# Optimization experiments

Measured on AMD Instinct MI355X. Metric: run time of the kernel, lower is better.

## Reference

```python
import jax, jax.numpy as jnp
import numpy as np

N, T, D, H = 4, 2048, 1024, 16
DK = D // H

def setup_inputs() -> dict:
    key = jax.random.key(0)
    k1, k2, k3 = jax.random.split(key, 3)
    z = jax.random.normal(k1, (N, T, D), dtype=jnp.float32)
    Wqkv = jax.random.normal(k2, (D, 3 * D), dtype=jnp.float32) * 0.01
    Wout = jax.random.normal(k3, (D, D), dtype=jnp.float32) * 0.01
    return {"z": z, "Wqkv": Wqkv, "Wout": Wout}

def reference(z, Wqkv, Wout):
    n, t, d = z.shape
    scale = DK ** -0.5
    qkv = z @ Wqkv  # [N,T,3D]
    q, k, v = jnp.split(qkv, 3, axis=-1)
    # [N,T,D] -> [N,H,T,dk]
    q = q.reshape(n, t, H, DK).transpose(0, 2, 1, 3)
    k = k.reshape(n, t, H, DK).transpose(0, 2, 1, 3)
    v = v.reshape(n, t, H, DK).transpose(0, 2, 1, 3)
    attn = jnp.einsum('nhqd,nhkd->nhqk', q, k) * scale
    causal = jnp.tril(jnp.ones((t, t), dtype=bool))
    attn = jnp.where(causal, attn, -jnp.inf)
    attn = jax.nn.softmax(attn, axis=-1)
    out = jnp.einsum('nhqk,nhkd->nhqd', attn, v)  # [N,H,T,dk]
    out = out.transpose(0, 2, 1, 3).reshape(n, t, d)
    return out @ Wout
```

## Files before the change

### kernel.cpp

```cpp
#include <hip/hip_runtime.h>
#include <hip/hip_bf16.h>

typedef __bf16 bf16;
typedef __bf16 bf16x8 __attribute__((ext_vector_type(8)));
typedef float f32x4 __attribute__((ext_vector_type(4)));

#define N_B 4
#define T_S 2048
#define D_M 1024
#define H_N 16
#define D_K 64
#define D3 3072
#define NEG_BIG (-1e30f)
#define QSCALE 0.18033688011112042f

#if __has_builtin(__builtin_amdgcn_exp2f)
#define EXP2(x) __builtin_amdgcn_exp2f(x)
#else
#define EXP2(x) exp2f(x)
#endif

__device__ __forceinline__ void gload_lds16(const bf16* g, bf16* l) {
    __builtin_amdgcn_global_load_lds((const __attribute__((address_space(1))) void*)g,
                                     (__attribute__((address_space(3))) void*)l, 16, 0, 0);
}

__device__ __forceinline__ bool probe_fp32(const void* p) {
    const unsigned int* w = (const unsigned int*)p;
    int weird = 0;
#pragma unroll
    for (int i = 0; i < 16; ++i) {
        unsigned int v = w[i];
        unsigned int e = (v >> 7) & 0xFFu;
        if ((v & 0xFFFFu) != 0u && (e < 100u || e > 140u)) weird++;
    }
    return weird >= 4;
}

__global__ __launch_bounds__(256) void prep(const void* __restrict__ z, bf16* __restrict__ zb,
                                            const void* __restrict__ Wqkv, bf16* __restrict__ WqkvT,
                                            const void* __restrict__ Wout, bf16* __restrict__ WoutT) {
    __shared__ bf16 tile[32][33];
    const int b = blockIdx.x;
    const int t = threadIdx.x;

    if (b < 4096) {
        const int i = (b * 256 + t) * 8;
        if (probe_fp32(z)) {
            const float* zf = (const float*)z;
            float4 u0 = *(const float4*)(zf + i);
            float4 u1 = *(const float4*)(zf + i + 4);
            union { uint4 q; bf16 h[8]; } pk;
            pk.h[0] = (bf16)u0.x; pk.h[1] = (bf16)u0.y;
            pk.h[2] = (bf16)u0.z; pk.h[3] = (bf16)u0.w;
            pk.h[4] = (bf16)u1.x; pk.h[5] = (bf16)u1.y;
            pk.h[6] = (bf16)u1.z; pk.h[7] = (bf16)u1.w;
            *(uint4*)(zb + i) = pk.q;
        } else {
            *(uint4*)(zb + i) = ((const uint4*)z)[b * 256 + t];
        }
        return;
    }

    const void* in; bf16* out; int R, C, c0, r0;
    if (b < 7168) {
        int idx = b - 4096;
        in = Wqkv; out = WqkvT; R = 1024; C = 3072;
        c0 = (idx % 96) * 32; r0 = (idx / 96) * 32;
    } else {
        int idx = b - 7168;
        in = Wout; out = WoutT; R = 1024; C = 1024;
        c0 = (idx & 31) * 32; r0 = (idx >> 5) * 32;
    }
    const int tx = t & 31, ty = t >> 5;
    if (probe_fp32(in)) {
        const float* inf_ = (const float*)in;
        for (int i = 0; i < 4; ++i)
            tile[ty + i * 8][tx] = (bf16)inf_[(size_t)(r0 + ty + i * 8) * C + c0 + tx];
    } else {
        const bf16* inb = (const bf16*)in;
        for (int i = 0; i < 4; ++i)
            tile[ty + i * 8][tx] = inb[(size_t)(r0 + ty + i * 8) * C + c0 + tx];
    }
    __syncthreads();
    for (int i = 0; i < 4; ++i)
        out[(size_t)(c0 + ty + i * 8) * R + r0 + tx] = tile[tx][ty + i * 8];
}

__global__ __launch_bounds__(512, 2) void gemmq(const bf16* __restrict__ A,
                                                const bf16* __restrict__ Bt,
                                                void* __restrict__ C,
                                                bf16* __restrict__ Kf,
                                                bf16* __restrict__ Vf,
                                                int M, int N, int K,
                                                int modeC, int nbx) {
    __shared__ bf16 As[2][256 * 64];
    __shared__ bf16 Bs[2][256 * 64];

    const int nwg = gridDim.x;
    const int per = nwg >> 3;
    const int b0 = blockIdx.x;
    const int bid = (b0 & 7) * per + (b0 >> 3);
    const int by = bid / nbx;
    const int bx = bid - by * nbx;
    const int m0 = by * 256, n0 = bx * 256;

    const int t = threadIdx.x;
    const int w = t >> 6, lane = t & 63, quad = lane >> 4, l15 = lane & 15;
    const int wr = (w >> 2) * 128;
    const int wc = (w & 3) * 64;
    const int sr = t >> 3;
    const int sg = ((t & 7) ^ (sr & 7)) * 8;
    const int xorL = (l15 & 7) * 8;
    const int ldsOff = w * 512;

    const bf16* ag0 = A + (size_t)(m0 + sr) * K + sg;
    const bf16* ag1 = A + (size_t)(m0 + 64 + sr) * K + sg;
    const bf16* ag2 = A + (size_t)(m0 + 128 + sr) * K + sg;
    const bf16* ag3 = A + (size_t)(m0 + 192 + sr) * K + sg;
    const bf16* bg0 = Bt + (size_t)(n0 + sr) * K + sg;
    const bf16* bg1 = Bt + (size_t)(n0 + 64 + sr) * K + sg;
    const bf16* bg2 = Bt + (size_t)(n0 + 128 + sr) * K + sg;
    const bf16* bg3 = Bt + (size_t)(n0 + 192 + sr) * K + sg;

    f32x4 acc[8][4];
    const f32x4 zero4 = {0.f, 0.f, 0.f, 0.f};
#pragma unroll
    for (int i = 0; i < 8; ++i)
#pragma unroll
        for (int j = 0; j < 4; ++j) acc[i][j] = zero4;

    const int nt = K >> 6;

    gload_lds16(ag0, &As[0][0 * 4096 + ldsOff]);
    gload_lds16(ag1, &As[0][1 * 4096 + ldsOff]);
    gload_lds16(ag2, &As[0][2 * 4096 + ldsOff]);
    gload_lds16(ag3, &As[0][3 * 4096 + ldsOff]);
    gload_lds16(bg0, &Bs[0][0 * 4096 + ldsOff]);
    gload_lds16(bg1, &Bs[0][1 * 4096 + ldsOff]);
    gload_lds16(bg2, &Bs[0][2 * 4096 + ldsOff]);
    gload_lds16(bg3, &Bs[0][3 * 4096 + ldsOff]);

    for (int tt = 0; tt < nt; ++tt) {
        const int s = tt & 1;
        __builtin_amdgcn_sched_barrier(0);
        if (tt + 1 < nt) {
            const int kn = (tt + 1) << 6;
            bf16* Ad = As[s ^ 1];
            bf16* Bd = Bs[s ^ 1];
            gload_lds16(ag0 + kn, Ad + 0 * 4096 + ldsOff);
            gload_lds16(ag1 + kn, Ad + 1 * 4096 + ldsOff);
            gload_lds16(ag2 + kn, Ad + 2 * 4096 + ldsOff);
            gload_lds16(ag3 + kn, Ad + 3 * 4096 + ldsOff);
            gload_lds16(bg0 + kn, Bd + 0 * 4096 + ldsOff);
            gload_lds16(bg1 + kn, Bd + 1 * 4096 + ldsOff);
            gload_lds16(bg2 + kn, Bd + 2 * 4096 + ldsOff);
            gload_lds16(bg3 + kn, Bd + 3 * 4096 + ldsOff);
            asm volatile("s_waitcnt vmcnt(8)" ::: "memory");
        } else {
            asm volatile("s_waitcnt vmcnt(0)" ::: "memory");
        }
        __builtin_amdgcn_sched_barrier(0);
        __builtin_amdgcn_s_barrier();
        __builtin_amdgcn_sched_barrier(0);

        const bf16* Ac = As[s];
        const bf16* Bc = Bs[s];

#pragma unroll
        for (int kk = 0; kk < 2; ++kk) {
            const int colOff = (kk * 32 + quad * 8) ^ xorL;
            bf16x8 bfv[4];
#pragma unroll
            for (int j = 0; j < 4; ++j)
                bfv[j] = *(const bf16x8*)(Bc + (wc + j * 16 + l15) * 64 + colOff);
            {
                bf16x8 af[4];
#pragma unroll
                for (int i = 0; i < 4; ++i)
                    af[i] = *(const bf16x8*)(Ac + (wr + i * 16 + l15) * 64 + colOff);
                __builtin_amdgcn_s_barrier();
                __builtin_amdgcn_s_setprio(1);
#pragma unroll
                for (int i = 0; i < 4; ++i)
#pragma unroll
                    for (int j = 0; j < 4; ++j)
                        acc[i][j] = __builtin_amdgcn_mfma_f32_16x16x32_bf16(af[i], bfv[j], acc[i][j], 0, 0, 0);
                __builtin_amdgcn_s_setprio(0);
                __builtin_amdgcn_s_barrier();
            }
            {
                bf16x8 af[4];
#pragma unroll
                for (int i = 0; i < 4; ++i)
                    af[i] = *(const bf16x8*)(Ac + (wr + 64 + i * 16 + l15) * 64 + colOff);
                __builtin_amdgcn_s_barrier();
                __builtin_amdgcn_s_setprio(1);
#pragma unroll
                for (int i = 0; i < 4; ++i)
#pragma unroll
                    for (int j = 0; j < 4; ++j)
                        acc[4 + i][j] = __builtin_amdgcn_mfma_f32_16x16x32_bf16(af[i], bfv[j], acc[4 + i][j], 0, 0, 0);
                __builtin_amdgcn_s_setprio(0);
                __builtin_amdgcn_s_barrier();
            }
        }
    }

    if (modeC == 1) {
        float* Cf = (float*)C;
        for (int ii = 0; ii < 8; ++ii) {
            int rowb = m0 + wr + ((ii >> 2) << 6) + ((ii & 3) << 4) + quad * 4;
            for (int fc = 0; fc < 4; ++fc)
                for (int r = 0; r < 4; ++r)
                    Cf[(size_t)(rowb + r) * N + (n0 + wc + fc * 16 + l15)] = acc[ii][fc][r];
        }
    } else if (n0 < 1024) {
        bf16* q = (bf16*)C;
        for (int ii = 0; ii < 8; ++ii) {
            int rowb = m0 + wr + ((ii >> 2) << 6) + ((ii & 3) << 4) + quad * 4;
            for (int fc = 0; fc < 4; ++fc)
                for (int r = 0; r < 4; ++r)
                    q[(size_t)(rowb + r) * 1024 + (n0 + wc + fc * 16 + l15)]
                        = (bf16)(acc[ii][fc][r] * QSCALE);
        }
    } else if (n0 < 2048) {
        for (int ii = 0; ii < 8; ++ii) {
            int rowb = m0 + wr + ((ii >> 2) << 6) + ((ii & 3) << 4) + quad * 4;
            int nb = rowb >> 11, tt = rowb & 2047;
            int kt = tt >> 6, f = (tt >> 4) & 3, l15k = tt & 15;
            for (int fc = 0; fc < 4; ++fc) {
                int col = n0 + wc + fc * 16 + l15 - 1024;
                int h = col >> 6, dk = col & 63;
                int ks = dk >> 5, qdk = (dk >> 3) & 3, j = dk & 7;
                size_t base = ((size_t)((nb * 16 + h) * 32 + kt) * 8 + ks * 4 + f) * 512 + j;
                for (int r = 0; r < 4; ++r)
                    Kf[base + (qdk * 16 + l15k + r) * 8] = (bf16)acc[ii][fc][r];
            }
        }
    } else {
        for (int ii = 0; ii < 8; ++ii) {
            int rowb = m0 + wr + ((ii >> 2) << 6) + ((ii & 3) << 4) + quad * 4;
            int nb = rowb >> 11, tt = rowb & 2047;
            int kt = tt >> 6, ks = (tt >> 5) & 1, qdv = (tt >> 3) & 3, j0 = tt & 7;
            for (int fc = 0; fc < 4; ++fc) {
                int col = n0 + wc + fc * 16 + l15 - 2048;
                int h = col >> 6, dl = col & 63;
                int fv = dl >> 4, l15v = dl & 15;
                union { ushort4 u; bf16 hh[4]; } pk;
                for (int r = 0; r < 4; ++r) pk.hh[r] = (bf16)acc[ii][fc][r];
                *(ushort4*)(Vf + ((size_t)((nb * 16 + h) * 32 + kt) * 8 + ks * 4 + fv) * 512
                            + (qdv * 16 + l15v) * 8 + j0) = pk.u;
            }
        }
    }
}

#define LDP 72
__global__ __launch_bounds__(256, 2) void attn_fused(const bf16* __restrict__ q,
                                                     const bf16* __restrict__ Kf,
                                                     const bf16* __restrict__ Vf,
                                                     bf16* __restrict__ attn_out) {
    __shared__ bf16 Pl[4 * 32 * LDP];

    const int b = blockIdx.x;
    const int head = b & 63;
    const int qp = b >> 6;
    const int n = head >> 4, h = head & 15;
    const int t = threadIdx.x;
    const int w = t >> 6, lane = t & 63, qd = lane >> 4, l15 = lane & 15;
    const int r = (w + qp + head) & 3;
    const int qt = (r < 2) ? qp : (31 - qp);
    const int q0w = qt * 64 + (r & 1) * 32;
    const size_t rowBase = (size_t)n * T_S;
    const bf16* KfH = Kf + (size_t)head * 32 * 4096;
    const bf16* VfH = Vf + (size_t)head * 32 * 4096;
    bf16* Plw = Pl + w * 32 * LDP;

    bf16x8 bQ[2][2];
#pragma unroll
    for (int qh = 0; qh < 2; ++qh)
#pragma unroll
        for (int ks = 0; ks < 2; ++ks)
            bQ[qh][ks] = *(const bf16x8*)(q + (rowBase + q0w + qh * 16 + l15) * 1024
                                          + h * 64 + ks * 32 + qd * 8);

    float l_lane[2] = {0.f, 0.f};
    f32x4 oacc[2][4];
    const f32x4 zero4 = {0.f, 0.f, 0.f, 0.f};
#pragma unroll
    for (int qh = 0; qh < 2; ++qh)
#pragma unroll
        for (int fd = 0; fd < 4; ++fd) oacc[qh][fd] = zero4;

    const int ktmax = (q0w + 31) >> 6;

    bf16x8 aK[2][4];
#pragma unroll
    for (int fr = 0; fr < 8; ++fr)
        aK[fr >> 2][fr & 3] = *(const bf16x8*)(KfH + fr * 512 + lane * 8);

    for (int kt = 0; kt <= ktmax; ++kt) {
        const int k0r = kt * 64;
        const bf16* VfT = VfH + (size_t)kt * 4096;

        bf16x8 aV[2][4];
#pragma unroll
        for (int fr = 0; fr < 8; ++fr)
            aV[fr >> 2][fr & 3] = *(const bf16x8*)(VfT + fr * 512 + lane * 8);

        f32x4 sacc[2][4];
#pragma unroll
        for (int qh = 0; qh < 2; ++qh)
#pragma unroll
            for (int fc = 0; fc < 4; ++fc) sacc[qh][fc] = zero4;
#pragma unroll
        for (int ks = 0; ks < 2; ++ks)
#pragma unroll
            for (int fc = 0; fc < 4; ++fc) {
                sacc[0][fc] = __builtin_amdgcn_mfma_f32_16x16x32_bf16(aK[ks][fc], bQ[0][ks], sacc[0][fc], 0, 0, 0);
                sacc[1][fc] = __builtin_amdgcn_mfma_f32_16x16x32_bf16(aK[ks][fc], bQ[1][ks], sacc[1][fc], 0, 0, 0);
            }

        if (kt < ktmax) {
            const bf16* KfN = KfH + (size_t)(kt + 1) * 4096;
#pragma unroll
            for (int fr = 0; fr < 8; ++fr)
                aK[fr >> 2][fr & 3] = *(const bf16x8*)(KfN + fr * 512 + lane * 8);
        }

        if (k0r + 63 > q0w) {
#pragma unroll
            for (int qh = 0; qh < 2; ++qh) {
                const int qq = q0w + qh * 16 + l15;
#pragma unroll
                for (int fc = 0; fc < 4; ++fc)
#pragma unroll
                    for (int rr = 0; rr < 4; ++rr)
                        if (k0r + fc * 16 + qd * 4 + rr > qq) sacc[qh][fc][rr] = NEG_BIG;
            }
        }

#pragma unroll
        for (int qh = 0; qh < 2; ++qh) {
            float rs = 0.f;
#pragma unroll
            for (int fc = 0; fc < 4; ++fc) {
                union { ushort4 u; bf16 hh[4]; } pk;
#pragma unroll
                for (int rr = 0; rr < 4; ++rr) {
                    float p = EXP2(sacc[qh][fc][rr]);
                    rs += p;
                    pk.hh[rr] = (bf16)p;
                }
                *(ushort4*)(Plw + (qh * 16 + l15) * LDP + fc * 16 + qd * 4) = pk.u;
            }
            l_lane[qh] += rs;
        }

#pragma unroll
        for (int ks = 0; ks < 2; ++ks) {
            bf16x8 bP0 = *(const bf16x8*)(Plw + l15 * LDP + ks * 32 + qd * 8);
            bf16x8 bP1 = *(const bf16x8*)(Plw + (16 + l15) * LDP + ks * 32 + qd * 8);
#pragma unroll
            for (int fd = 0; fd < 4; ++fd) {
                oacc[0][fd] = __builtin_amdgcn_mfma_f32_16x16x32_bf16(aV[ks][fd], bP0, oacc[0][fd], 0, 0, 0);
                oacc[1][fd] = __builtin_amdgcn_mfma_f32_16x16x32_bf16(aV[ks][fd], bP1, oacc[1][fd], 0, 0, 0);
            }
        }
    }

#pragma unroll
    for (int qh = 0; qh < 2; ++qh) {
        float l = l_lane[qh];
        l += __shfl_xor(l, 16, 64);
        l += __shfl_xor(l, 32, 64);
        float inv = 1.f / l;
#pragma unroll
        for (int fd = 0; fd < 4; ++fd) {
            union { ushort4 u; bf16 hh[4]; } pk;
#pragma unroll
            for (int rr = 0; rr < 4; ++rr) pk.hh[rr] = (bf16)(oacc[qh][fd][rr] * inv);
            *(ushort4*)(attn_out + (rowBase + q0w + qh * 16 + l15) * D_M
                        + h * D_K + fd * 16 + qd * 4) = pk.u;
        }
    }
}

extern "C" void kernel_launch(void* const* d_in, const int* in_sizes, int n_in,
                              void* d_out, int out_size, void* d_ws, size_t ws_size,
                              hipStream_t stream) {
    const void* z    = d_in[0];
    const void* Wqkv = d_in[1];
    const void* Wout = d_in[2];

    char* ws = (char*)d_ws;
    bf16* q     = (bf16*)(ws + 256);
    bf16* attn  = (bf16*)(ws + 256 + 16777216);
    bf16* zb    = attn;
    bf16* WqkvT = (bf16*)(ws + 256 + 2 * 16777216);
    bf16* WoutT = (bf16*)(ws + 256 + 2 * 16777216 + 6291456);

    bf16* Kf = (bf16*)d_out;
    bf16* Vf = Kf + 8388608;

    prep<<<dim3(8192), 256, 0, stream>>>(z, zb, Wqkv, WqkvT, Wout, WoutT);

    gemmq<<<dim3(384), 512, 0, stream>>>(
        zb, WqkvT, q, Kf, Vf, N_B * T_S, D3, D_M, 2, 12);

    attn_fused<<<dim3(64 * 16), 256, 0, stream>>>(q, Kf, Vf, attn);

    gemmq<<<dim3(128), 512, 0, stream>>>(
        attn, WoutT, d_out, Kf, Vf, N_B * T_S, D_M, D_M, 1, 4);
}
```

Baseline: 264.6 us.

## Split GEMM tile loads across phases, template BN, add MFMA priority in attention

Measured after the change: 245.7 us. -7.1%, faster.

```diff
diff --git a/kernel.cpp b/kernel.cpp
--- a/kernel.cpp
+++ b/kernel.cpp
@@ -87,15 +87,17 @@
         out[(size_t)(c0 + ty + i * 8) * R + r0 + tx] = tile[tx][ty + i * 8];
 }
 
-__global__ __launch_bounds__(512, 2) void gemmq(const bf16* __restrict__ A,
-                                                const bf16* __restrict__ Bt,
-                                                void* __restrict__ C,
-                                                bf16* __restrict__ Kf,
-                                                bf16* __restrict__ Vf,
-                                                int M, int N, int K,
-                                                int modeC, int nbx) {
+template<int BN>
+__global__ __launch_bounds__(512, 2) void gemm8p(const bf16* __restrict__ A,
+                                                 const bf16* __restrict__ Bt,
+                                                 void* __restrict__ C,
+                                                 bf16* __restrict__ Kf,
+                                                 bf16* __restrict__ Vf,
+                                                 int M, int N, int K,
+                                                 int modeC, int nbx) {
+    constexpr int NBF = BN / 64;
     __shared__ bf16 As[2][256 * 64];
-    __shared__ bf16 Bs[2][256 * 64];
+    __shared__ bf16 Bs[2][BN * 64];
 
     const int nwg = gridDim.x;
     const int per = nwg >> 3;
@@ -103,115 +105,146 @@
     const int bid = (b0 & 7) * per + (b0 >> 3);
     const int by = bid / nbx;
     const int bx = bid - by * nbx;
-    const int m0 = by * 256, n0 = bx * 256;
+    const int m0 = by * 256, n0 = bx * BN;
 
     const int t = threadIdx.x;
     const int w = t >> 6, lane = t & 63, quad = lane >> 4, l15 = lane & 15;
     const int wr = (w >> 2) * 128;
-    const int wc = (w & 3) * 64;
+    const int wc = (w & 3) * (BN / 4);
     const int sr = t >> 3;
     const int sg = ((t & 7) ^ (sr & 7)) * 8;
     const int xorL = (l15 & 7) * 8;
     const int ldsOff = w * 512;
 
-    const bf16* ag0 = A + (size_t)(m0 + sr) * K + sg;
-    const bf16* ag1 = A + (size_t)(m0 + 64 + sr) * K + sg;
-    const bf16* ag2 = A + (size_t)(m0 + 128 + sr) * K + sg;
-    const bf16* ag3 = A + (size_t)(m0 + 192 + sr) * K + sg;
-    const bf16* bg0 = Bt + (size_t)(n0 + sr) * K + sg;
-    const bf16* bg1 = Bt + (size_t)(n0 + 64 + sr) * K + sg;
-    const bf16* bg2 = Bt + (size_t)(n0 + 128 + sr) * K + sg;
-    const bf16* bg3 = Bt + (size_t)(n0 + 192 + sr) * K + sg;
-
-    f32x4 acc[8][4];
+    const bf16* ag[4] = { A + (size_t)(m0 + sr) * K + sg,
+                          A + (size_t)(m0 + 64 + sr) * K + sg,
+                          A + (size_t)(m0 + 128 + sr) * K + sg,
+                          A + (size_t)(m0 + 192 + sr) * K + sg };
+    const bf16* bg[4] = { Bt + (size_t)(n0 + sr) * K + sg,
+                          Bt + (size_t)(n0 + 64 + sr) * K + sg,
+                          (BN == 256) ? Bt + (size_t)(n0 + 128 + sr) * K + sg : Bt,
+                          (BN == 256) ? Bt + (size_t)(n0 + 192 + sr) * K + sg : Bt };
+
+    f32x4 acc[8][NBF];
     const f32x4 zero4 = {0.f, 0.f, 0.f, 0.f};
 #pragma unroll
     for (int i = 0; i < 8; ++i)
 #pragma unroll
-        for (int j = 0; j < 4; ++j) acc[i][j] = zero4;
+        for (int j = 0; j < NBF; ++j) acc[i][j] = zero4;
 
     const int nt = K >> 6;
 
-    gload_lds16(ag0, &As[0][0 * 4096 + ldsOff]);
-    gload_lds16(ag1, &As[0][1 * 4096 + ldsOff]);
-    gload_lds16(ag2, &As[0][2 * 4096 + ldsOff]);
-    gload_lds16(ag3, &As[0][3 * 4096 + ldsOff]);
-    gload_lds16(bg0, &Bs[0][0 * 4096 + ldsOff]);
-    gload_lds16(bg1, &Bs[0][1 * 4096 + ldsOff]);
-    gload_lds16(bg2, &Bs[0][2 * 4096 + ldsOff]);
-    gload_lds16(bg3, &Bs[0][3 * 4096 + ldsOff]);
+#define STA_(buf, c, kt) gload_lds16(ag[c] + ((kt) << 6), &As[buf][(c) * 4096 + ldsOff])
+#define STB_(buf, c, kt) gload_lds16(bg[c] + ((kt) << 6), &Bs[buf][(c) * 4096 + ldsOff])
+#define BAR1_ do { __builtin_amdgcn_sched_barrier(0); __builtin_amdgcn_s_barrier(); \
+        asm volatile("s_waitcnt lgkmcnt(0)" ::: "memory"); \
+        __builtin_amdgcn_sched_barrier(0); } while (0)
+#define BAR2_ do { __builtin_amdgcn_sched_barrier(0); __builtin_amdgcn_s_barrier(); \
+        __builtin_amdgcn_sched_barrier(0); } while (0)
+
+    STB_(0, 0, 0); STB_(0, 1, 0); STA_(0, 0, 0); STA_(0, 2, 0);
+    if constexpr (BN == 256) { STB_(0, 2, 0); STB_(0, 3, 0); }
+    STA_(0, 1, 0); STA_(0, 3, 0);
+    if (nt > 1) {
+        STB_(1, 0, 1); STB_(1, 1, 1); STA_(1, 0, 1); STA_(1, 2, 1);
+        asm volatile("s_waitcnt vmcnt(6)" ::: "memory");
+    } else {
+        asm volatile("s_waitcnt vmcnt(0)" ::: "memory");
+    }
+    BAR2_;
 
     for (int tt = 0; tt < nt; ++tt) {
-        const int s = tt & 1;
-        __builtin_amdgcn_sched_barrier(0);
+        const int s = tt & 1, os = s ^ 1;
+        const bf16* Ac = &As[s][0];
+        const bf16* Bc = &Bs[s][0];
+        const int co0 = (quad * 8) ^ xorL;
+        const int co1 = (32 + quad * 8) ^ xorL;
+        bf16x8 af[4], bfv[NBF];
+
+#pragma unroll
+        for (int j = 0; j < NBF; ++j)
+            bfv[j] = *(const bf16x8*)(Bc + (wc + j * 16 + l15) * 64 + co0);
+#pragma unroll
+        for (int i = 0; i < 4; ++i)
+            af[i] = *(const bf16x8*)(Ac + (wr + i * 16 + l15) * 64 + co0);
         if (tt + 1 < nt) {
-            const int kn = (tt + 1) << 6;
-            bf16* Ad = As[s ^ 1];
-            bf16* Bd = Bs[s ^ 1];
-            gload_lds16(ag0 + kn, Ad + 0 * 4096 + ldsOff);
-            gload_lds16(ag1 + kn, Ad + 1 * 4096 + ldsOff);
-            gload_lds16(ag2 + kn, Ad + 2 * 4096 + ldsOff);
-            gload_lds16(ag3 + kn, Ad + 3 * 4096 + ldsOff);
-            gload_lds16(bg0 + kn, Bd + 0 * 4096 + ldsOff);
-            gload_lds16(bg1 + kn, Bd + 1 * 4096 + ldsOff);
-            gload_lds16(bg2 + kn, Bd + 2 * 4096 + ldsOff);
-            gload_lds16(bg3 + kn, Bd + 3 * 4096 + ldsOff);
-            asm volatile("s_waitcnt vmcnt(8)" ::: "memory");
+            if constexpr (BN == 256) { STB_(os, 2, tt + 1); STB_(os, 3, tt + 1); }
+            STA_(os, 1, tt + 1); STA_(os, 3, tt + 1);
+        }
+        if (tt == nt - 1) {
+            asm volatile("s_waitcnt vmcnt(0)" ::: "memory");
         } else {
-            asm volatile("s_waitcnt vmcnt(0)" ::: "memory");
-        }
-        __builtin_amdgcn_sched_barrier(0);
-        __builtin_amdgcn_s_barrier();
-        __builtin_amdgcn_sched_barrier(0);
-
-        const bf16* Ac = As[s];
-        const bf16* Bc = Bs[s];
-
-#pragma unroll
-        for (int kk = 0; kk < 2; ++kk) {
-            const int colOff = (kk * 32 + quad * 8) ^ xorL;
-            bf16x8 bfv[4];
-#pragma unroll
-            for (int j = 0; j < 4; ++j)
-                bfv[j] = *(const bf16x8*)(Bc + (wc + j * 16 + l15) * 64 + colOff);
-            {
-                bf16x8 af[4];
-#pragma unroll
-                for (int i = 0; i < 4; ++i)
-                    af[i] = *(const bf16x8*)(Ac + (wr + i * 16 + l15) * 64 + colOff);
-                __builtin_amdgcn_s_barrier();
-                __builtin_amdgcn_s_setprio(1);
-#pragma unroll
-                for (int i = 0; i < 4; ++i)
-#pragma unroll
-                    for (int j = 0; j < 4; ++j)
-                        acc[i][j] = __builtin_amdgcn_mfma_f32_16x16x32_bf16(af[i], bfv[j], acc[i][j], 0, 0, 0);
-                __builtin_amdgcn_s_setprio(0);
-                __builtin_amdgcn_s_barrier();
-            }
-            {
-                bf16x8 af[4];
-#pragma unroll
-                for (int i = 0; i < 4; ++i)
-                    af[i] = *(const bf16x8*)(Ac + (wr + 64 + i * 16 + l15) * 64 + colOff);
-                __builtin_amdgcn_s_barrier();
-                __builtin_amdgcn_s_setprio(1);
-#pragma unroll
-                for (int i = 0; i < 4; ++i)
-#pragma unroll
-                    for (int j = 0; j < 4; ++j)
-                        acc[4 + i][j] = __builtin_amdgcn_mfma_f32_16x16x32_bf16(af[i], bfv[j], acc[4 + i][j], 0, 0, 0);
-                __builtin_amdgcn_s_setprio(0);
-                __builtin_amdgcn_s_barrier();
-            }
-        }
-    }
+            if constexpr (BN == 256) { asm volatile("s_waitcnt vmcnt(8)" ::: "memory"); }
+            else                     { asm volatile("s_waitcnt vmcnt(6)" ::: "memory"); }
+        }
+        BAR1_;
+        __builtin_amdgcn_s_setprio(1);
+#pragma unroll
+        for (int i = 0; i < 4; ++i)
+#pragma unroll
+            for (int j = 0; j < NBF; ++j)
+                acc[i][j] = __builtin_amdgcn_mfma_f32_16x16x32_bf16(af[i], bfv[j], acc[i][j], 0, 0, 0);
+        __builtin_amdgcn_s_setprio(0);
+        BAR2_;
+
+#pragma unroll
+        for (int i = 0; i < 4; ++i)
+            af[i] = *(const bf16x8*)(Ac + (wr + 64 + i * 16 + l15) * 64 + co0);
+        BAR1_;
+        __builtin_amdgcn_s_setprio(1);
+#pragma unroll
+        for (int i = 0; i < 4; ++i)
+#pragma unroll
+            for (int j = 0; j < NBF; ++j)
+                acc[4 + i][j] = __builtin_amdgcn_mfma_f32_16x16x32_bf16(af[i], bfv[j], acc[4 + i][j], 0, 0, 0);
+        __builtin_amdgcn_s_setprio(0);
+        BAR2_;
+
+#pragma unroll
+        for (int j = 0; j < NBF; ++j)
+            bfv[j] = *(const bf16x8*)(Bc + (wc + j * 16 + l15) * 64 + co1);
+#pragma unroll
+        for (int i = 0; i < 4; ++i)
+            af[i] = *(const bf16x8*)(Ac + (wr + i * 16 + l15) * 64 + co1);
+        BAR1_;
+        __builtin_amdgcn_s_setprio(1);
+#pragma unroll
+        for (int i = 0; i < 4; ++i)
+#pragma unroll
+            for (int j = 0; j < NBF; ++j)
+                acc[i][j] = __builtin_amdgcn_mfma_f32_16x16x32_bf16(af[i], bfv[j], acc[i][j], 0, 0, 0);
+        __builtin_amdgcn_s_setprio(0);
+        BAR2_;
+
+#pragma unroll
+        for (int i = 0; i < 4; ++i)
+            af[i] = *(const bf16x8*)(Ac + (wr + 64 + i * 16 + l15) * 64 + co1);
+        if (tt + 2 < nt) {
+            STB_(s, 0, tt + 2); STB_(s, 1, tt + 2); STA_(s, 0, tt + 2); STA_(s, 2, tt + 2);
+            asm volatile("s_waitcnt vmcnt(6)" ::: "memory");
+        } else if (tt + 2 == nt) {
+            asm volatile("s_waitcnt vmcnt(2)" ::: "memory");
+        }
+        BAR1_;
+        __builtin_amdgcn_s_setprio(1);
+#pragma unroll
+        for (int i = 0; i < 4; ++i)
+#pragma unroll
+            for (int j = 0; j < NBF; ++j)
+                acc[4 + i][j] = __builtin_amdgcn_mfma_f32_16x16x32_bf16(af[i], bfv[j], acc[4 + i][j], 0, 0, 0);
+        __builtin_amdgcn_s_setprio(0);
+        BAR2_;
+    }
+#undef STA_
+#undef STB_
+#undef BAR1_
+#undef BAR2_
 
     if (modeC == 1) {
         float* Cf = (float*)C;
         for (int ii = 0; ii < 8; ++ii) {
             int rowb = m0 + wr + ((ii >> 2) << 6) + ((ii & 3) << 4) + quad * 4;
-            for (int fc = 0; fc < 4; ++fc)
+            for (int fc = 0; fc < NBF; ++fc)
                 for (int r = 0; r < 4; ++r)
                     Cf[(size_t)(rowb + r) * N + (n0 + wc + fc * 16 + l15)] = acc[ii][fc][r];
         }
@@ -219,7 +252,7 @@
         bf16* q = (bf16*)C;
         for (int ii = 0; ii < 8; ++ii) {
             int rowb = m0 + wr + ((ii >> 2) << 6) + ((ii & 3) << 4) + quad * 4;
-            for (int fc = 0; fc < 4; ++fc)
+            for (int fc = 0; fc < NBF; ++fc)
                 for (int r = 0; r < 4; ++r)
                     q[(size_t)(rowb + r) * 1024 + (n0 + wc + fc * 16 + l15)]
                         = (bf16)(acc[ii][fc][r] * QSCALE);
@@ -227,9 +260,9 @@
     } else if (n0 < 2048) {
         for (int ii = 0; ii < 8; ++ii) {
             int rowb = m0 + wr + ((ii >> 2) << 6) + ((ii & 3) << 4) + quad * 4;
-            int nb = rowb >> 11, tt = rowb & 2047;
-            int kt = tt >> 6, f = (tt >> 4) & 3, l15k = tt & 15;
-            for (int fc = 0; fc < 4; ++fc) {
+            int nb = rowb >> 11, ttr = rowb & 2047;
+            int kt = ttr >> 6, f = (ttr >> 4) & 3, l15k = ttr & 15;
+            for (int fc = 0; fc < NBF; ++fc) {
                 int col = n0 + wc + fc * 16 + l15 - 1024;
                 int h = col >> 6, dk = col & 63;
                 int ks = dk >> 5, qdk = (dk >> 3) & 3, j = dk & 7;
@@ -241,9 +274,9 @@
     } else {
         for (int ii = 0; ii < 8; ++ii) {
             int rowb = m0 + wr + ((ii >> 2) << 6) + ((ii & 3) << 4) + quad * 4;
-            int nb = rowb >> 11, tt = rowb & 2047;
-            int kt = tt >> 6, ks = (tt >> 5) & 1, qdv = (tt >> 3) & 3, j0 = tt & 7;
-            for (int fc = 0; fc < 4; ++fc) {
+            int nb = rowb >> 11, ttr = rowb & 2047;
+            int kt = ttr >> 6, ks = (ttr >> 5) & 1, qdv = (ttr >> 3) & 3, j0 = ttr & 7;
+            for (int fc = 0; fc < NBF; ++fc) {
                 int col = n0 + wc + fc * 16 + l15 - 2048;
                 int h = col >> 6, dl = col & 63;
                 int fv = dl >> 4, l15v = dl & 15;
@@ -314,6 +347,7 @@
         for (int qh = 0; qh < 2; ++qh)
 #pragma unroll
             for (int fc = 0; fc < 4; ++fc) sacc[qh][fc] = zero4;
+        __builtin_amdgcn_s_setprio(1);
 #pragma unroll
         for (int ks = 0; ks < 2; ++ks)
 #pragma unroll
@@ -321,6 +355,7 @@
                 sacc[0][fc] = __builtin_amdgcn_mfma_f32_16x16x32_bf16(aK[ks][fc], bQ[0][ks], sacc[0][fc], 0, 0, 0);
                 sacc[1][fc] = __builtin_amdgcn_mfma_f32_16x16x32_bf16(aK[ks][fc], bQ[1][ks], sacc[1][fc], 0, 0, 0);
             }
+        __builtin_amdgcn_s_setprio(0);
 
         if (kt < ktmax) {
             const bf16* KfN = KfH + (size_t)(kt + 1) * 4096;
@@ -358,6 +393,7 @@
             l_lane[qh] += rs;
         }
 
+        __builtin_amdgcn_s_setprio(1);
 #pragma unroll
         for (int ks = 0; ks < 2; ++ks) {
             bf16x8 bP0 = *(const bf16x8*)(Plw + l15 * LDP + ks * 32 + qd * 8);
@@ -368,6 +404,7 @@
                 oacc[1][fd] = __builtin_amdgcn_mfma_f32_16x16x32_bf16(aV[ks][fd], bP1, oacc[1][fd], 0, 0, 0);
             }
         }
+        __builtin_amdgcn_s_setprio(0);
     }
 
 #pragma unroll
@@ -406,11 +443,11 @@
 
     prep<<<dim3(8192), 256, 0, stream>>>(z, zb, Wqkv, WqkvT, Wout, WoutT);
 
-    gemmq<<<dim3(384), 512, 0, stream>>>(
+    gemm8p<256><<<dim3(384), 512, 0, stream>>>(
         zb, WqkvT, q, Kf, Vf, N_B * T_S, D3, D_M, 2, 12);
 
     attn_fused<<<dim3(64 * 16), 256, 0, stream>>>(q, Kf, Vf, attn);
 
-    gemmq<<<dim3(128), 512, 0, stream>>>(
-        attn, WoutT, d_out, Kf, Vf, N_B * T_S, D_M, D_M, 1, 4);
-}
+    gemm8p<128><<<dim3(256), 512, 0, stream>>>(
+        attn, WoutT, d_out, Kf, Vf, N_B * T_S, D_M, D_M, 1, 8);
+}
```
